# Kernel tuning notes

Measured on AMD Instinct MI355X. Metric: run time of the kernel, lower is better.

## Reference

```python
import jax, jax.numpy as jnp
import numpy as np

HIDDEN = 1024
N_HEADS = 16
HEAD_DIM = HIDDEN // N_HEADS  # 64
B, N = 2, 2048
SCALE = HIDDEN ** (-0.5)  # NOTE: original scales by full hidden_size, not head_dim


def setup_inputs() -> dict:
    key = jax.random.key(0)
    k1, k2 = jax.random.split(key)
    hidden_states = jax.random.normal(k1, (B, N, HIDDEN), dtype=jnp.float32)
    attention_mask = jnp.ones((B, N), dtype=jnp.int32)
    # per-head no-bias Linear(hidden -> 3*head_dim), stacked: [h, hidden, 3*head_dim]
    W_qkv = jax.random.normal(k2, (N_HEADS, HIDDEN, 3 * HEAD_DIM), dtype=jnp.float32) * (HIDDEN ** -0.5)
    return {"hidden_states": hidden_states, "attention_mask": attention_mask, "W_qkv": W_qkv}


def reference(hidden_states, attention_mask, W_qkv):
    # qkv: [b, h, n, 3*d]
    qkv = jnp.einsum('bnD,hDe->bhne', hidden_states, W_qkv)
    q, k, v = jnp.split(qkv, 3, axis=-1)  # each [b, h, n, d]
    scores = jnp.einsum('bhid,bhjd->bhij', q, k) * SCALE
    mask = attention_mask[:, None, None, :] == 0  # [b,1,1,n]
    scores = jnp.where(mask, -jnp.inf, scores)
    attn = jax.nn.softmax(scores, axis=-1)
    out = jnp.einsum('bhij,bhjd->bhid', attn, v)  # [b, h, n, d]
    # rearrange 'b h n d -> b n (h d)'
    return jnp.transpose(out, (0, 2, 1, 3)).reshape(out.shape[0], out.shape[2], -1)
```

## Files before the change

### kernel.cpp

```cpp
#include <hip/hip_runtime.h>
#include <hip/hip_bf16.h>


#define NH   16
#define HD   64
#define SEQ  2048
#define HID  1024
#define E3   192
#define QSCALE 0.04508422017f
#define MBIAS  -43.2808512f

typedef __attribute__((ext_vector_type(8))) short short8;
typedef __attribute__((ext_vector_type(4))) float f32x4;
typedef unsigned short ushort_t;

#define MFMA16(a, b, c) __builtin_amdgcn_mfma_f32_16x16x32_bf16((a), (b), (c), 0, 0, 0)

#if __has_builtin(__builtin_amdgcn_exp2f)
#define EXP2(x) __builtin_amdgcn_exp2f(x)
#else
#define EXP2(x) exp2f(x)
#endif

static __device__ __forceinline__ ushort_t f2bf(float x) {
    unsigned u = __builtin_bit_cast(unsigned, x);
    unsigned r = u + 0x7fff + ((u >> 16) & 1);
    return (ushort_t)(r >> 16);
}

static __device__ __forceinline__ unsigned pack_trunc(float hi, float lo) {
#if __has_builtin(__builtin_amdgcn_perm)
    return __builtin_amdgcn_perm(__builtin_bit_cast(unsigned, hi),
                                 __builtin_bit_cast(unsigned, lo), 0x07060302u);
#else
    return (__builtin_bit_cast(unsigned, hi) & 0xffff0000u) |
           (__builtin_bit_cast(unsigned, lo) >> 16);
#endif
}

static __device__ __forceinline__ void load_lds16(const void* g, void* l) {
    __builtin_amdgcn_global_load_lds(
        (__attribute__((address_space(1))) void*)(g),
        (__attribute__((address_space(3))) void*)(l), 16, 0, 0);
}

__global__ __launch_bounds__(256) void k_cvt_x(const void* __restrict__ Xv,
                                               ushort_t* __restrict__ Xb,
                                               int* __restrict__ flagp) {
    __shared__ int cnt;
    if (threadIdx.x == 0) cnt = 0;
    __syncthreads();
    const unsigned* X32 = (const unsigned*)Xv;
    if (threadIdx.x < 64) {
        unsigned u = X32[(size_t)blockIdx.x * 2048 + threadIdx.x * 32 + 7];
        int bexp = (u >> 7) & 0xFF;
        if (bexp >= 0x68 && bexp <= 0x90) atomicAdd(&cnt, 1);
    }
    __syncthreads();
    const int isf32 = (cnt < 32);
    if (blockIdx.x == 0 && threadIdx.x == 0) *flagp = isf32;

    const size_t base = ((size_t)blockIdx.x * 256 + threadIdx.x) * 16;
    if (isf32) {
        const float* Xf = (const float*)Xv;
        ushort_t tmp[16];
#pragma unroll
        for (int c = 0; c < 4; ++c) {
            float4 v = *(const float4*)(Xf + base + c * 4);
            tmp[c * 4 + 0] = f2bf(v.x); tmp[c * 4 + 1] = f2bf(v.y);
            tmp[c * 4 + 2] = f2bf(v.z); tmp[c * 4 + 3] = f2bf(v.w);
        }
        *(float4*)(Xb + base)     = ((const float4*)tmp)[0];
        *(float4*)(Xb + base + 8) = ((const float4*)tmp)[1];
    } else {
        const ushort_t* Xh = (const ushort_t*)Xv;
        *(float4*)(Xb + base)     = *(const float4*)(Xh + base);
        *(float4*)(Xb + base + 8) = *(const float4*)(Xh + base + 8);
    }
}

__global__ __launch_bounds__(256) void k_cvt_w(const void* __restrict__ Wv,
                                               ushort_t* __restrict__ Wt,
                                               const int* __restrict__ flagp) {
    __shared__ ushort_t tile[64][72];
    const int isf32 = *flagp;
    const int h  = blockIdx.x;
    const int dt = blockIdx.y;
    const int et = blockIdx.z;
    const int D0 = dt * 64, e0 = et * 64;
    const int t  = threadIdx.x;
#pragma unroll
    for (int r = 0; r < 2; ++r) {
        int row = r * 32 + (t >> 3);
        int col = (t & 7) * 8;
        size_t base = ((size_t)(h * HID + D0 + row)) * E3 + e0 + col;
        if (isf32) {
            const float* Wf = (const float*)Wv;
            float4 a = *(const float4*)(Wf + base);
            float4 c = *(const float4*)(Wf + base + 4);
            tile[row][col + 0] = f2bf(a.x); tile[row][col + 1] = f2bf(a.y);
            tile[row][col + 2] = f2bf(a.z); tile[row][col + 3] = f2bf(a.w);
            tile[row][col + 4] = f2bf(c.x); tile[row][col + 5] = f2bf(c.y);
            tile[row][col + 6] = f2bf(c.z); tile[row][col + 7] = f2bf(c.w);
        } else {
            *(float4*)&tile[row][col] = *(const float4*)((const ushort_t*)Wv + base);
        }
    }
    __syncthreads();
#pragma unroll
    for (int r = 0; r < 2; ++r) {
        int erow = r * 32 + (t >> 3);
        int dcol = (t & 7) * 8;
        ushort_t vals[8];
#pragma unroll
        for (int i = 0; i < 8; ++i) vals[i] = tile[dcol + i][erow];
        *(float4*)(Wt + ((size_t)(h * E3 + e0 + erow)) * HID + D0 + dcol) = *(float4*)vals;
    }
}

__global__ __launch_bounds__(256) void k_qkv(const ushort_t* __restrict__ Xb,
                                             const ushort_t* __restrict__ Wt,
                                             ushort_t* __restrict__ Qb,
                                             ushort_t* __restrict__ Kb,
                                             ushort_t* __restrict__ Vtb) {
    __shared__ __align__(16) ushort_t smem[2 * 128 * 64];
    ushort_t* Xl = smem;
    ushort_t* Wl = smem + 128 * 64;

    const int e0 = blockIdx.x * 128;
    const int m0 = blockIdx.y * 128;
    const int b  = m0 >> 11;
    const int n0 = m0 & 2047;
    const int t = threadIdx.x;
    const int w = t >> 6, lane = t & 63, l15 = lane & 15, quad = lane >> 4;
    const int wrow0 = (w & 1) * 64, wcol0 = (w >> 1) * 64;
    const int srow = lane >> 3;
    const int scb  = (lane & 7) ^ srow;

    f32x4 acc[4][4];
#pragma unroll
    for (int i = 0; i < 4; ++i)
#pragma unroll
        for (int j = 0; j < 4; ++j) acc[i][j] = (f32x4){0.f, 0.f, 0.f, 0.f};

    for (int k0 = 0; k0 < HID; k0 += 64) {
        __syncthreads();
#pragma unroll
        for (int cc = 0; cc < 4; ++cc) {
            const int ch  = w * 4 + cc;
            const int row = ch * 8 + srow;
            load_lds16(Xb + (size_t)(m0 + row) * HID + k0 + scb * 8, &Xl[ch * 512]);
            load_lds16(Wt + (size_t)(e0 + row) * HID + k0 + scb * 8, &Wl[ch * 512]);
        }
        __syncthreads();
#pragma unroll
        for (int kh = 0; kh < 2; ++kh) {
            short8 af[4], bfm[4];
#pragma unroll
            for (int i = 0; i < 4; ++i) {
                const int r = wrow0 + i * 16 + l15;
                af[i] = *(const short8*)&Xl[r * 64 + ((kh * 4 + quad) ^ (r & 7)) * 8];
            }
#pragma unroll
            for (int j = 0; j < 4; ++j) {
                const int r = wcol0 + j * 16 + l15;
                bfm[j] = *(const short8*)&Wl[r * 64 + ((kh * 4 + quad) ^ (r & 7)) * 8];
            }
#pragma unroll
            for (int i = 0; i < 4; ++i)
#pragma unroll
                for (int j = 0; j < 4; ++j)
                    acc[i][j] = MFMA16(af[i], bfm[j], acc[i][j]);
        }
    }

    ushort_t* Vbuf = smem;
    __syncthreads();
#pragma unroll
    for (int i = 0; i < 4; ++i) {
#pragma unroll
        for (int j = 0; j < 4; ++j) {
            const int E0v = e0 + wcol0 + j * 16;
            const int hh  = E0v / 192;
            const int r0  = E0v - hh * 192;
            const int bh  = b * NH + hh;
            const int nb  = n0 + wrow0 + i * 16 + quad * 4;
            if (r0 < 64) {
                const int e = r0 + l15;
#pragma unroll
                for (int reg = 0; reg < 4; ++reg)
                    Qb[((size_t)bh * SEQ + nb + reg) * HD + e] = f2bf(acc[i][j][reg] * QSCALE);
            } else if (r0 < 128) {
                const int e = r0 - 64 + l15;
#pragma unroll
                for (int reg = 0; reg < 4; ++reg)
                    Kb[((size_t)bh * SEQ + nb + reg) * HD + e] = f2bf(acc[i][j][reg]);
            } else {
                const int d  = r0 - 128 + l15;
                const int nl = wrow0 + i * 16 + quad * 4;
#pragma unroll
                for (int reg = 0; reg < 4; ++reg)
                    Vbuf[d * 136 + nl + reg] = f2bf(acc[i][j][reg]);
            }
        }
    }
    const int m3 = blockIdx.x % 3;
    if (m3 != 0) {
        __syncthreads();
        const int hv  = (e0 + ((m3 == 1) ? 0 : 64)) / 192;
        const int bhv = b * NH + hv;
        const int dr = t >> 2, part = t & 3;
        size_t dst = ((size_t)bhv * HD + dr) * SEQ + n0 + part * 32;
#pragma unroll
        for (int c = 0; c < 4; ++c) {
            float4 v = *(const float4*)&Vbuf[dr * 136 + part * 32 + c * 8];
            *(float4*)(Vtb + dst + c * 8) = v;
        }
    }
}

__global__ __launch_bounds__(512) void k_attn(const ushort_t* __restrict__ Qb,
                                              const ushort_t* __restrict__ Kb,
                                              const ushort_t* __restrict__ Vtb,
                                              const int* __restrict__ mask,
                                              void* __restrict__ outv,
                                              const int* __restrict__ flagp) {
    __shared__ __align__(16) char smem_raw[75776];
    ushort_t* Pl    = (ushort_t*)(smem_raw + 49152);
    float*    biasl = (float*)(smem_raw + 67584);

    const int isf32 = *flagp;
    const int q0 = blockIdx.x * 128;
    const int bh = blockIdx.y;
    const int b  = bh >> 4, h = bh & 15;
    const int t  = threadIdx.x;
    const int w  = t >> 6, lane = t & 63, l15 = lane & 15, quad = lane >> 4;
    const int srow = lane >> 3;
    const int scb  = (lane & 7) ^ srow;
    const int row8 = w * 8 + srow;

    const f32x4 zero4 = {0.f, 0.f, 0.f, 0.f};

#pragma unroll
    for (int tj = 0; tj < 2; ++tj) {
        ushort_t* kb = (ushort_t*)(smem_raw + tj * 16384);
        ushort_t* vb = kb + 4096;
        load_lds16(Kb  + ((size_t)bh * SEQ + tj * 64 + row8) * HD + scb * 8, &kb[w * 512]);
        load_lds16(Vtb + ((size_t)bh * HD + row8) * SEQ + tj * 64 + scb * 8, &vb[w * 512]);
    }

    int lm = 0;
    for (int i = t; i < SEQ; i += 512) {
        int mv = mask[b * SEQ + i];
        biasl[i] = mv ? 0.0f : MBIAS;
        lm |= (mv == 0);
    }
    const int qrow = q0 + w * 16 + l15;
    short8 qa0 = *(const short8*)(Qb + ((size_t)bh * SEQ + qrow) * HD + quad * 8);
    short8 qa1 = *(const short8*)(Qb + ((size_t)bh * SEQ + qrow) * HD + 32 + quad * 8);

    const int use_bias = __syncthreads_or(lm);

    f32x4 o[4];
#pragma unroll
    for (int mt = 0; mt < 4; ++mt) o[mt] = zero4;
    float l_r = 0.f;

    for (int j0 = 0; j0 < SEQ; j0 += 64) {
        const int idx = (j0 >> 6) % 3;
        if (j0 + 64 < SEQ) { asm volatile("s_waitcnt vmcnt(2)" ::: "memory"); }
        else               { asm volatile("s_waitcnt vmcnt(0)" ::: "memory"); }
        __builtin_amdgcn_s_barrier();
        asm volatile("" ::: "memory");
        if (j0 + 128 < SEQ) {
            ushort_t* kb = (ushort_t*)(smem_raw + ((idx + 2) % 3) * 16384);
            ushort_t* vb = kb + 4096;
            load_lds16(Kb  + ((size_t)bh * SEQ + j0 + 128 + row8) * HD + scb * 8, &kb[w * 512]);
            load_lds16(Vtb + ((size_t)bh * HD + row8) * SEQ + j0 + 128 + scb * 8, &vb[w * 512]);
        }
        ushort_t* kb = (ushort_t*)(smem_raw + idx * 16384);
        ushort_t* vb = kb + 4096;

        f32x4 s[4];
#pragma unroll
        for (int jt = 0; jt < 4; ++jt) {
            const int rk = jt * 16 + l15;
            short8 kb0 = *(const short8*)&kb[rk * 64 + ((quad)     ^ (rk & 7)) * 8];
            short8 kb1 = *(const short8*)&kb[rk * 64 + ((4 + quad) ^ (rk & 7)) * 8];
            s[jt] = MFMA16(kb0, qa0, zero4);
            s[jt] = MFMA16(kb1, qa1, s[jt]);
        }
        if (use_bias) {
#pragma unroll
            for (int jt = 0; jt < 4; ++jt) {
                float4 bj = *(const float4*)&biasl[j0 + jt * 16 + quad * 4];
#pragma unroll
                for (int reg = 0; reg < 4; ++reg)
                    s[jt][reg] += ((const float*)&bj)[reg];
            }
        }

#pragma unroll
        for (int jt = 0; jt < 4; ++jt) {
            float p0 = EXP2(s[jt][0]);
            float p1 = EXP2(s[jt][1]);
            float p2 = EXP2(s[jt][2]);
            float p3 = EXP2(s[jt][3]);
            l_r += (p0 + p1) + (p2 + p3);
            uint2 u;
            u.x = pack_trunc(p1, p0);
            u.y = pack_trunc(p3, p2);
            *(uint2*)&Pl[(w * 16 + l15) * 72 + jt * 16 + quad * 4] = u;
        }
        short8 pb0 = *(const short8*)&Pl[(w * 16 + l15) * 72 + quad * 8];
        short8 pb1 = *(const short8*)&Pl[(w * 16 + l15) * 72 + 32 + quad * 8];
#pragma unroll
        for (int mt = 0; mt < 4; ++mt) {
            const int rv = mt * 16 + l15;
            short8 va0 = *(const short8*)&vb[rv * 64 + ((quad)     ^ (rv & 7)) * 8];
            short8 va1 = *(const short8*)&vb[rv * 64 + ((4 + quad) ^ (rv & 7)) * 8];
            o[mt] = MFMA16(va0, pb0, o[mt]);
            o[mt] = MFMA16(va1, pb1, o[mt]);
        }
    }

    l_r += __shfl_xor(l_r, 16);
    l_r += __shfl_xor(l_r, 32);
    const float rinv = 1.0f / l_r;

    __syncthreads();
    const int r = t >> 2, part = t & 3;
    if (!isf32) {
        ushort_t* Ol = (ushort_t*)smem_raw;
#pragma unroll
        for (int mt = 0; mt < 4; ++mt) {
            uint2 u;
            u.x = (unsigned)f2bf(o[mt][0] * rinv) | ((unsigned)f2bf(o[mt][1] * rinv) << 16);
            u.y = (unsigned)f2bf(o[mt][2] * rinv) | ((unsigned)f2bf(o[mt][3] * rinv) << 16);
            *(uint2*)&Ol[(w * 16 + l15) * 72 + mt * 16 + quad * 4] = u;
        }
        __syncthreads();
        float4 v0 = *(const float4*)&Ol[r * 72 + part * 16];
        float4 v1 = *(const float4*)&Ol[r * 72 + part * 16 + 8];
        ushort_t* outp = (ushort_t*)outv;
        size_t dst = ((size_t)b * SEQ + q0 + r) * HID + h * HD + part * 16;
        *(float4*)(outp + dst)     = v0;
        *(float4*)(outp + dst + 8) = v1;
    } else {
        float* Olf = (float*)smem_raw;
#pragma unroll
        for (int mt = 0; mt < 4; ++mt)
#pragma unroll
            for (int reg = 0; reg < 4; ++reg)
                Olf[(w * 16 + l15) * 68 + mt * 16 + quad * 4 + reg] = o[mt][reg] * rinv;
        __syncthreads();
        float* outp = (float*)outv;
        size_t dst = ((size_t)b * SEQ + q0 + r) * HID + h * HD + part * 16;
#pragma unroll
        for (int c = 0; c < 4; ++c) {
            float4 v = *(const float4*)&Olf[r * 68 + part * 16 + c * 4];
            *(float4*)(outp + dst + c * 4) = v;
        }
    }
}

extern "C" void kernel_launch(void* const* d_in, const int* in_sizes, int n_in,
                              void* d_out, int out_size, void* d_ws, size_t ws_size,
                              hipStream_t stream) {
    const void* X    = d_in[0];
    const int*  mask = (const int*)d_in[1];
    const void* W    = d_in[2];

    char* ws = (char*)d_ws;
    ushort_t* Qb    = (ushort_t*)(ws);
    ushort_t* Kb    = (ushort_t*)(ws + 8388608);
    ushort_t* Vtb   = (ushort_t*)(ws + 16777216);
    ushort_t* Wtb   = (ushort_t*)(ws + 25165824);
    int*      flagp = (int*)(ws + 31457280);
    ushort_t* Xb    = (ushort_t*)d_out;

    k_cvt_x<<<1024, 256, 0, stream>>>(X, Xb, flagp);
    k_cvt_w<<<dim3(16, 16, 3), 256, 0, stream>>>(W, Wtb, flagp);
    k_qkv<<<dim3(24, 32), 256, 0, stream>>>(Xb, Wtb, Qb, Kb, Vtb);
    k_attn<<<dim3(16, 32), 512, 0, stream>>>(Qb, Kb, Vtb, mask, d_out, flagp);
}
```

Measured before the change: 180.0 us.

## Switch attention to 32x32x16 MFMA with register-resident P via permlane32 swap

Rewrites the attention kernel to use 32x32x16 bf16 MFMA tiles: each of 4 waves now owns 32 query rows instead of 8 waves with 16 rows. The softmax probabilities are repacked between the S and PV MFMAs with v_permlane32_swap instead of a round trip through LDS, so the P shared buffer and its loads and stores go away. The block shrinks to 256 threads and uses less LDS. Each wave now loads more of the K/V tile and holds more accumulator registers, which may lower occupancy or latency hiding.

```diff
diff --git a/kernel.cpp b/kernel.cpp
--- a/kernel.cpp
+++ b/kernel.cpp
@@ -12,9 +12,11 @@
 
 typedef __attribute__((ext_vector_type(8))) short short8;
 typedef __attribute__((ext_vector_type(4))) float f32x4;
+typedef __attribute__((ext_vector_type(16))) float f32x16;
 typedef unsigned short ushort_t;
 
 #define MFMA16(a, b, c) __builtin_amdgcn_mfma_f32_16x16x32_bf16((a), (b), (c), 0, 0, 0)
+#define MFMA32(a, b, c) __builtin_amdgcn_mfma_f32_32x32x16_bf16((a), (b), (c), 0, 0, 0)
 
 #if __has_builtin(__builtin_amdgcn_exp2f)
 #define EXP2(x) __builtin_amdgcn_exp2f(x)
@@ -219,148 +221,185 @@
     }
 }
 
-__global__ __launch_bounds__(512) void k_attn(const ushort_t* __restrict__ Qb,
+
+#define SMPACK(sv, h0v, h1v)                                                  \
+    {                                                                         \
+        _Pragma("unroll")                                                     \
+        for (int g = 0; g < 4; ++g) {                                         \
+            float p0 = EXP2(sv[4*g+0]); float p1 = EXP2(sv[4*g+1]);           \
+            float p2 = EXP2(sv[4*g+2]); float p3 = EXP2(sv[4*g+3]);           \
+            l_r += (p0 + p1) + (p2 + p3);                                     \
+            unsigned a0 = pack_trunc(p1, p0), a1 = pack_trunc(p3, p2);        \
+            unsigned b0 = a0, b1 = a1;                                        \
+            asm volatile("v_permlane32_swap_b32 %0, %1" : "+v"(a0), "+v"(b0));\
+            asm volatile("v_permlane32_swap_b32 %0, %1" : "+v"(a1), "+v"(b1));\
+            h0v[g*2+0] = a0; h1v[g*2+0] = b0;                                 \
+            h0v[g*2+1] = a1; h1v[g*2+1] = b1;                                 \
+        }                                                                     \
+    }
+
+#define MAKE_PB(dst, h0v, h1v, GB)                                            \
+    {                                                                         \
+        unsigned w0_ = hi ? h0v[(GB+1)*2+0] : h0v[(GB)*2+0];                  \
+        unsigned w1_ = hi ? h0v[(GB+1)*2+1] : h0v[(GB)*2+1];                  \
+        unsigned w2_ = hi ? h1v[(GB+1)*2+0] : h1v[(GB)*2+0];                  \
+        unsigned w3_ = hi ? h1v[(GB+1)*2+1] : h1v[(GB)*2+1];                  \
+        uint4 u_ = {w0_, w1_, w2_, w3_};                                      \
+        dst = __builtin_bit_cast(short8, u_);                                 \
+    }
+
+__global__ __launch_bounds__(256) void k_attn(const ushort_t* __restrict__ Qb,
                                               const ushort_t* __restrict__ Kb,
                                               const ushort_t* __restrict__ Vtb,
                                               const int* __restrict__ mask,
                                               void* __restrict__ outv,
                                               const int* __restrict__ flagp) {
-    __shared__ __align__(16) char smem_raw[75776];
-    ushort_t* Pl    = (ushort_t*)(smem_raw + 49152);
-    float*    biasl = (float*)(smem_raw + 67584);
+    __shared__ __align__(16) char smem_raw[57344];
+    float* biasl = (float*)(smem_raw + 49152);
 
     const int isf32 = *flagp;
     const int q0 = blockIdx.x * 128;
     const int bh = blockIdx.y;
     const int b  = bh >> 4, h = bh & 15;
     const int t  = threadIdx.x;
-    const int w  = t >> 6, lane = t & 63, l15 = lane & 15, quad = lane >> 4;
+    const int w  = t >> 6, lane = t & 63;
+    const int c31 = lane & 31, hi = lane >> 5;
     const int srow = lane >> 3;
     const int scb  = (lane & 7) ^ srow;
-    const int row8 = w * 8 + srow;
-
-    const f32x4 zero4 = {0.f, 0.f, 0.f, 0.f};
+    const int rx7  = c31 & 7;
 
 #pragma unroll
     for (int tj = 0; tj < 2; ++tj) {
         ushort_t* kb = (ushort_t*)(smem_raw + tj * 16384);
         ushort_t* vb = kb + 4096;
-        load_lds16(Kb  + ((size_t)bh * SEQ + tj * 64 + row8) * HD + scb * 8, &kb[w * 512]);
-        load_lds16(Vtb + ((size_t)bh * HD + row8) * SEQ + tj * 64 + scb * 8, &vb[w * 512]);
+        load_lds16(Kb  + ((size_t)bh * SEQ + tj * 64 + w * 16 + srow)     * HD + scb * 8, &kb[(w * 2 + 0) * 512]);
+        load_lds16(Kb  + ((size_t)bh * SEQ + tj * 64 + w * 16 + 8 + srow) * HD + scb * 8, &kb[(w * 2 + 1) * 512]);
+        load_lds16(Vtb + ((size_t)bh * HD + w * 16 + srow)     * SEQ + tj * 64 + scb * 8, &vb[(w * 2 + 0) * 512]);
+        load_lds16(Vtb + ((size_t)bh * HD + w * 16 + 8 + srow) * SEQ + tj * 64 + scb * 8, &vb[(w * 2 + 1) * 512]);
     }
 
     int lm = 0;
-    for (int i = t; i < SEQ; i += 512) {
+    for (int i = t; i < SEQ; i += 256) {
         int mv = mask[b * SEQ + i];
         biasl[i] = mv ? 0.0f : MBIAS;
         lm |= (mv == 0);
     }
-    const int qrow = q0 + w * 16 + l15;
-    short8 qa0 = *(const short8*)(Qb + ((size_t)bh * SEQ + qrow) * HD + quad * 8);
-    short8 qa1 = *(const short8*)(Qb + ((size_t)bh * SEQ + qrow) * HD + 32 + quad * 8);
+    const int qrow = q0 + w * 32 + c31;
+    short8 qB[4];
+#pragma unroll
+    for (int ds = 0; ds < 4; ++ds)
+        qB[ds] = *(const short8*)(Qb + ((size_t)bh * SEQ + qrow) * HD + ds * 16 + hi * 8);
 
     const int use_bias = __syncthreads_or(lm);
 
-    f32x4 o[4];
-#pragma unroll
-    for (int mt = 0; mt < 4; ++mt) o[mt] = zero4;
+    f32x16 oa, ob;
+#pragma unroll
+    for (int i = 0; i < 16; ++i) { oa[i] = 0.f; ob[i] = 0.f; }
     float l_r = 0.f;
 
     for (int j0 = 0; j0 < SEQ; j0 += 64) {
         const int idx = (j0 >> 6) % 3;
-        if (j0 + 64 < SEQ) { asm volatile("s_waitcnt vmcnt(2)" ::: "memory"); }
+        if (j0 + 64 < SEQ) { asm volatile("s_waitcnt vmcnt(4)" ::: "memory"); }
         else               { asm volatile("s_waitcnt vmcnt(0)" ::: "memory"); }
         __builtin_amdgcn_s_barrier();
         asm volatile("" ::: "memory");
         if (j0 + 128 < SEQ) {
-            ushort_t* kb = (ushort_t*)(smem_raw + ((idx + 2) % 3) * 16384);
-            ushort_t* vb = kb + 4096;
-            load_lds16(Kb  + ((size_t)bh * SEQ + j0 + 128 + row8) * HD + scb * 8, &kb[w * 512]);
-            load_lds16(Vtb + ((size_t)bh * HD + row8) * SEQ + j0 + 128 + scb * 8, &vb[w * 512]);
+            ushort_t* kb2 = (ushort_t*)(smem_raw + ((idx + 2) % 3) * 16384);
+            ushort_t* vb2 = kb2 + 4096;
+            load_lds16(Kb  + ((size_t)bh * SEQ + j0 + 128 + w * 16 + srow)     * HD + scb * 8, &kb2[(w * 2 + 0) * 512]);
+            load_lds16(Kb  + ((size_t)bh * SEQ + j0 + 128 + w * 16 + 8 + srow) * HD + scb * 8, &kb2[(w * 2 + 1) * 512]);
+            load_lds16(Vtb + ((size_t)bh * HD + w * 16 + srow)     * SEQ + j0 + 128 + scb * 8, &vb2[(w * 2 + 0) * 512]);
+            load_lds16(Vtb + ((size_t)bh * HD + w * 16 + 8 + srow) * SEQ + j0 + 128 + scb * 8, &vb2[(w * 2 + 1) * 512]);
         }
         ushort_t* kb = (ushort_t*)(smem_raw + idx * 16384);
         ushort_t* vb = kb + 4096;
 
-        f32x4 s[4];
-#pragma unroll
-        for (int jt = 0; jt < 4; ++jt) {
-            const int rk = jt * 16 + l15;
-            short8 kb0 = *(const short8*)&kb[rk * 64 + ((quad)     ^ (rk & 7)) * 8];
-            short8 kb1 = *(const short8*)&kb[rk * 64 + ((4 + quad) ^ (rk & 7)) * 8];
-            s[jt] = MFMA16(kb0, qa0, zero4);
-            s[jt] = MFMA16(kb1, qa1, s[jt]);
+        f32x16 s0, s1;
+#pragma unroll
+        for (int i = 0; i < 16; ++i) { s0[i] = 0.f; s1[i] = 0.f; }
+#pragma unroll
+        for (int ds = 0; ds < 4; ++ds) {
+            short8 kf0 = *(const short8*)&kb[(c31)      * 64 + ((2 * ds + hi) ^ rx7) * 8];
+            short8 kf1 = *(const short8*)&kb[(32 + c31) * 64 + ((2 * ds + hi) ^ rx7) * 8];
+            s0 = MFMA32(kf0, qB[ds], s0);
+            s1 = MFMA32(kf1, qB[ds], s1);
         }
         if (use_bias) {
 #pragma unroll
-            for (int jt = 0; jt < 4; ++jt) {
-                float4 bj = *(const float4*)&biasl[j0 + jt * 16 + quad * 4];
-#pragma unroll
-                for (int reg = 0; reg < 4; ++reg)
-                    s[jt][reg] += ((const float*)&bj)[reg];
-            }
-        }
-
-#pragma unroll
-        for (int jt = 0; jt < 4; ++jt) {
-            float p0 = EXP2(s[jt][0]);
-            float p1 = EXP2(s[jt][1]);
-            float p2 = EXP2(s[jt][2]);
-            float p3 = EXP2(s[jt][3]);
-            l_r += (p0 + p1) + (p2 + p3);
-            uint2 u;
-            u.x = pack_trunc(p1, p0);
-            u.y = pack_trunc(p3, p2);
-            *(uint2*)&Pl[(w * 16 + l15) * 72 + jt * 16 + quad * 4] = u;
-        }
-        short8 pb0 = *(const short8*)&Pl[(w * 16 + l15) * 72 + quad * 8];
-        short8 pb1 = *(const short8*)&Pl[(w * 16 + l15) * 72 + 32 + quad * 8];
-#pragma unroll
-        for (int mt = 0; mt < 4; ++mt) {
-            const int rv = mt * 16 + l15;
-            short8 va0 = *(const short8*)&vb[rv * 64 + ((quad)     ^ (rv & 7)) * 8];
-            short8 va1 = *(const short8*)&vb[rv * 64 + ((4 + quad) ^ (rv & 7)) * 8];
-            o[mt] = MFMA16(va0, pb0, o[mt]);
-            o[mt] = MFMA16(va1, pb1, o[mt]);
-        }
-    }
-
-    l_r += __shfl_xor(l_r, 16);
+            for (int g = 0; g < 4; ++g) {
+                float4 bj0 = *(const float4*)&biasl[j0 +      8 * g + 4 * hi];
+                float4 bj1 = *(const float4*)&biasl[j0 + 32 + 8 * g + 4 * hi];
+                s0[4*g+0] += bj0.x; s0[4*g+1] += bj0.y; s0[4*g+2] += bj0.z; s0[4*g+3] += bj0.w;
+                s1[4*g+0] += bj1.x; s1[4*g+1] += bj1.y; s1[4*g+2] += bj1.z; s1[4*g+3] += bj1.w;
+            }
+        }
+
+        unsigned h0a[8], h1a[8], h0b[8], h1b[8];
+        SMPACK(s0, h0a, h1a);
+        SMPACK(s1, h0b, h1b);
+
+#pragma unroll
+        for (int jt = 0; jt < 2; ++jt) {
+#pragma unroll
+            for (int c13 = 0; c13 < 2; ++c13) {
+                short8 pb;
+                if (jt == 0) { MAKE_PB(pb, h0a, h1a, 2 * c13); }
+                else         { MAKE_PB(pb, h0b, h1b, 2 * c13); }
+                const int cbase = 2 * (jt * 2 + c13) + hi;
+                short8 va0 = *(const short8*)&vb[(c31)      * 64 + (cbase ^ rx7) * 8];
+                short8 va1 = *(const short8*)&vb[(32 + c31) * 64 + (cbase ^ rx7) * 8];
+                oa = MFMA32(va0, pb, oa);
+                ob = MFMA32(va1, pb, ob);
+            }
+        }
+    }
+
     l_r += __shfl_xor(l_r, 32);
     const float rinv = 1.0f / l_r;
 
     __syncthreads();
-    const int r = t >> 2, part = t & 3;
+    const int qlr = w * 32 + c31;
+    const int r = t >> 1, part = t & 1;
     if (!isf32) {
         ushort_t* Ol = (ushort_t*)smem_raw;
 #pragma unroll
-        for (int mt = 0; mt < 4; ++mt) {
-            uint2 u;
-            u.x = (unsigned)f2bf(o[mt][0] * rinv) | ((unsigned)f2bf(o[mt][1] * rinv) << 16);
-            u.y = (unsigned)f2bf(o[mt][2] * rinv) | ((unsigned)f2bf(o[mt][3] * rinv) << 16);
-            *(uint2*)&Ol[(w * 16 + l15) * 72 + mt * 16 + quad * 4] = u;
+        for (int dt = 0; dt < 2; ++dt) {
+            const f32x16 ov = dt ? ob : oa;
+#pragma unroll
+            for (int g = 0; g < 4; ++g) {
+                const int d0 = dt * 32 + 8 * g + 4 * hi;
+                uint2 u;
+                u.x = (unsigned)f2bf(ov[4*g+0] * rinv) | ((unsigned)f2bf(ov[4*g+1] * rinv) << 16);
+                u.y = (unsigned)f2bf(ov[4*g+2] * rinv) | ((unsigned)f2bf(ov[4*g+3] * rinv) << 16);
+                *(uint2*)&Ol[qlr * 72 + d0] = u;
+            }
         }
         __syncthreads();
-        float4 v0 = *(const float4*)&Ol[r * 72 + part * 16];
-        float4 v1 = *(const float4*)&Ol[r * 72 + part * 16 + 8];
         ushort_t* outp = (ushort_t*)outv;
-        size_t dst = ((size_t)b * SEQ + q0 + r) * HID + h * HD + part * 16;
-        *(float4*)(outp + dst)     = v0;
-        *(float4*)(outp + dst + 8) = v1;
+        size_t dst = ((size_t)b * SEQ + q0 + r) * HID + h * HD + part * 32;
+#pragma unroll
+        for (int c = 0; c < 4; ++c)
+            *(float4*)(outp + dst + c * 8) = *(const float4*)&Ol[r * 72 + part * 32 + c * 8];
     } else {
         float* Olf = (float*)smem_raw;
 #pragma unroll
-        for (int mt = 0; mt < 4; ++mt)
-#pragma unroll
-            for (int reg = 0; reg < 4; ++reg)
-                Olf[(w * 16 + l15) * 68 + mt * 16 + quad * 4 + reg] = o[mt][reg] * rinv;
+        for (int dt = 0; dt < 2; ++dt) {
+            const f32x16 ov = dt ? ob : oa;
+#pragma unroll
+            for (int g = 0; g < 4; ++g) {
+                const int d0 = dt * 32 + 8 * g + 4 * hi;
+                float4 fv;
+                fv.x = ov[4*g+0] * rinv; fv.y = ov[4*g+1] * rinv;
+                fv.z = ov[4*g+2] * rinv; fv.w = ov[4*g+3] * rinv;
+                *(float4*)&Olf[qlr * 68 + d0] = fv;
+            }
+        }
         __syncthreads();
         float* outp = (float*)outv;
-        size_t dst = ((size_t)b * SEQ + q0 + r) * HID + h * HD + part * 16;
-#pragma unroll
-        for (int c = 0; c < 4; ++c) {
-            float4 v = *(const float4*)&Olf[r * 68 + part * 16 + c * 4];
-            *(float4*)(outp + dst + c * 4) = v;
-        }
+        size_t dst = ((size_t)b * SEQ + q0 + r) * HID + h * HD + part * 32;
+#pragma unroll
+        for (int c = 0; c < 8; ++c)
+            *(float4*)(outp + dst + c * 4) = *(const float4*)&Olf[r * 68 + part * 32 + c * 4];
     }
 }
 
@@ -382,5 +421,5 @@
     k_cvt_x<<<1024, 256, 0, stream>>>(X, Xb, flagp);
     k_cvt_w<<<dim3(16, 16, 3), 256, 0, stream>>>(W, Wtb, flagp);
     k_qkv<<<dim3(24, 32), 256, 0, stream>>>(Xb, Wtb, Qb, Kb, Vtb);
-    k_attn<<<dim3(16, 32), 512, 0, stream>>>(Qb, Kb, Vtb, mask, d_out, flagp);
-}
+    k_attn<<<dim3(16, 32), 256, 0, stream>>>(Qb, Kb, Vtb, mask, d_out, flagp);
+}
```

Measured after the change: 186.6 us. +3.6%, slower.
